# Kernel tuning notes

Measured on AMD Instinct MI355X. Metric: run time of the kernel, lower is better.

Reference implementation:

```python
import jax, jax.numpy as jnp
import numpy as np

STEP_SIZE = 0.3333
MAX_STEPS = 8          # >= ceil(max(2*sigma)/step); extra iterations have k==0 (no-op)
TANGENT_DIRECTION = True


def _bilinear_sample(img, p):
    # img: [B,C,H,W], p: [B,2,H,W] normalized coords in [0,1] (x=width, y=height)
    B, C, H, W = img.shape
    fx = p[:, 0] * W - 0.5   # [B,H,W] pixel-center convention
    fy = p[:, 1] * H - 0.5
    x0 = jnp.floor(fx)
    y0 = jnp.floor(fy)
    wx = (fx - x0)[:, None]  # [B,1,H,W]
    wy = (fy - y0)[:, None]
    x0i = jnp.clip(x0.astype(jnp.int32), 0, W - 1)
    x1i = jnp.clip(x0i + 1, 0, W - 1)
    y0i = jnp.clip(y0.astype(jnp.int32), 0, H - 1)
    y1i = jnp.clip(y0i + 1, 0, H - 1)
    gather = jax.vmap(lambda im, yi, xi: im[:, yi, xi])  # per-batch gather -> [B,C,H,W]
    v00 = gather(img, y0i, x0i)
    v01 = gather(img, y0i, x1i)
    v10 = gather(img, y1i, x0i)
    v11 = gather(img, y1i, x1i)
    return (v00 * (1 - wx) + v01 * wx) * (1 - wy) + (v10 * (1 - wx) + v11 * wx) * wy


def _p_start(H, W, dtype):
    xs = (jnp.arange(W, dtype=dtype) + 0.5) / W
    ys = (jnp.arange(H, dtype=dtype) + 0.5) / H
    px = jnp.broadcast_to(xs[None, :], (H, W))
    py = jnp.broadcast_to(ys[:, None], (H, W))
    return jnp.stack([px, py])[None]  # [1,2,H,W]


def _perp(t):
    return jnp.concatenate([t[:, 1:2], -t[:, 0:1]], axis=1)


def _forward(x, tangent, sigma):
    B, C, H, W = x.shape
    dt = x.dtype
    factor = min(H, W) / 1024.0          # input_size_factor relative to 1024 base res
    sigma = sigma * factor               # [B,1,1,1]
    half_width = 2.0 * sigma
    two_sigma2 = 2.0 * sigma * sigma
    step = jnp.asarray(1.0 / (STEP_SIZE * factor), dtype=dt)
    tex = jnp.array([W, H], dtype=dt).reshape(1, 2, 1, 1)
    p0 = _p_start(H, W, dt)

    def one_pass(direction):
        v = direction if TANGENT_DIRECTION else _perp(direction)
        p = p0 + v / tex
        r = jnp.broadcast_to(step, (B, 1, 1, 1))
        c = jnp.zeros_like(x)
        s = jnp.zeros((B, 1, H, W), dt)

        def body(carry, _):
            c, s, v, p, r = carry
            k = jnp.exp(-r * r / two_sigma2)                 # [B,1,1,1]
            k = jnp.where(r < half_width, k, 0.0)
            inb = ((p[:, 0:1] >= 0.0) & (p[:, 0:1] < 1.0) &
                   (p[:, 1:2] >= 0.0) & (p[:, 1:2] < 1.0))   # [B,1,H,W]
            k = jnp.where(inb, k, 0.0)                        # [B,1,H,W]
            c = c + _bilinear_sample(x, p) * k
            s = s + k
            tf = _bilinear_sample(tangent, p)                 # [B,2,H,W]
            if not TANGENT_DIRECTION:
                tf = _perp(tf)
            vt = jnp.sum(v * tf, axis=1, keepdims=True)
            tf = jnp.where(vt < 0.0, -tf, tf)                 # keep marching direction coherent
            return (c, s, tf, p + tf / tex, r + step), None

        (c, s, _, _, _), _ = jax.lax.scan(body, (c, s, v, p, r), None, length=MAX_STEPS)
        return c, s

    c1, s1 = one_pass(tangent)
    c2, s2 = one_pass(-tangent)
    return (x + c1 + c2) / (1.0 + s1 + s2)


def setup_inputs() -> dict:
    key = jax.random.key(0)
    k1, k2, k3 = jax.random.split(key, 3)
    B, C, H, W = 2, 3, 1024, 1024
    x = jax.random.uniform(k1, (B, C, H, W), dtype=jnp.float32)
    t = jax.random.normal(k2, (B, 2, H, W), dtype=jnp.float32)
    t = t / (jnp.sqrt(jnp.sum(t * t, axis=1, keepdims=True)) + 1e-6)  # unit tangent field
    sigma = 2.0 + 4.0 * jax.random.uniform(k3, (B, 1, 1, 1), dtype=jnp.float32)
    return {"x": x, "tangent": t, "sigma": sigma}


def reference(x, tangent, sigma):
    return _forward(x, tangent, sigma)
```

## Files before the change

### kernel.cpp

```cpp
#include <hip/hip_runtime.h>
#include <hip/hip_fp16.h>


#define HH 1024
#define WW 1024
#define CC 3
#define BB 2
#define NPIX (HH * WW)

#define TS 32
#define HALO_LO 5
#define NWIN 43
#define NREC (NWIN * NWIN)

__device__ __forceinline__ unsigned pk_f16x2(float a, float b) {
    __half2 h = __floats2half2_rn(a, b);
    return *(const unsigned*)&h;
}
__device__ __forceinline__ float2 unpk_f16x2(unsigned u) {
    __half2 h = *(const __half2*)&u;
    return __half22float2(h);
}

template <bool BORDER>
__device__ __forceinline__ float4 march_pixel(
    const uint4* __restrict__ win, int win_x0, int win_y0,
    int ix, int iy, float t0x, float t0y,
    float half_width, float inv_two_sigma2, float step)
{
    const float invT = 1.0f / 1024.0f;
    float acc0 = 0.f, acc1 = 0.f, acc2 = 0.f, accs = 0.f;

    float vx[2], vy[2], px[2], py[2];
    vx[0] = t0x;  vy[0] = t0y;
    vx[1] = -t0x; vy[1] = -t0y;
    const float p0x = ((float)ix + 0.5f) * invT;
    const float p0y = ((float)iy + 0.5f) * invT;
    px[0] = p0x + vx[0] * invT;  py[0] = p0y + vy[0] * invT;
    px[1] = p0x + vx[1] * invT;  py[1] = p0y + vy[1] * invT;

    float r = step;
    for (int it = 0; it < 8; ++it) {
        if (!(r < half_width)) break;
        const float k = __expf(-r * r * inv_two_sigma2);

        #pragma unroll
        for (int c = 0; c < 2; ++c) {
            const float fx = px[c] * 1024.0f - 0.5f;
            const float fy = py[c] * 1024.0f - 0.5f;
            const float x0f = floorf(fx);
            const float y0f = floorf(fy);
            const float wx = fx - x0f;
            const float wy = fy - y0f;

            int jx0, jx1, jy0, jy1;
            if (BORDER) {
                int x0i = (int)x0f, y0i = (int)y0f;
                x0i = min(max(x0i, 0), WW - 1);
                y0i = min(max(y0i, 0), HH - 1);
                const int x1i = min(x0i + 1, WW - 1);
                const int y1i = min(y0i + 1, HH - 1);
                jx0 = x0i - win_x0; jx1 = x1i - win_x0;
                jy0 = y0i - win_y0; jy1 = y1i - win_y0;
            } else {
                jx0 = (int)x0f - win_x0; jx1 = jx0 + 1;
                jy0 = (int)y0f - win_y0; jy1 = jy0 + 1;
            }

            const uint4 q00 = win[jy0 * NWIN + jx0];
            const uint4 q01 = win[jy0 * NWIN + jx1];
            const uint4 q10 = win[jy1 * NWIN + jx0];
            const uint4 q11 = win[jy1 * NWIN + jx1];

            const float wxm = 1.f - wx;
            const float wym = 1.f - wy;
            const float w00 = wxm * wym, w01 = wx * wym;
            const float w10 = wxm * wy,  w11 = wx * wy;

            float tfx = __uint_as_float(q00.x) * w00 + __uint_as_float(q01.x) * w01
                      + __uint_as_float(q10.x) * w10 + __uint_as_float(q11.x) * w11;
            float tfy = __uint_as_float(q00.y) * w00 + __uint_as_float(q01.y) * w01
                      + __uint_as_float(q10.y) * w10 + __uint_as_float(q11.y) * w11;

            bool inb = true;
            if (BORDER)
                inb = (px[c] >= 0.f) && (px[c] < 1.f) &&
                      (py[c] >= 0.f) && (py[c] < 1.f);
            if (inb) {
                const float2 a00 = unpk_f16x2(q00.z);
                const float2 a01 = unpk_f16x2(q01.z);
                const float2 a10 = unpk_f16x2(q10.z);
                const float2 a11 = unpk_f16x2(q11.z);
                const float2 b00 = unpk_f16x2(q00.w);
                const float2 b01 = unpk_f16x2(q01.w);
                const float2 b10 = unpk_f16x2(q10.w);
                const float2 b11 = unpk_f16x2(q11.w);
                acc0 += k * (a00.x * w00 + a01.x * w01 + a10.x * w10 + a11.x * w11);
                acc1 += k * (a00.y * w00 + a01.y * w01 + a10.y * w10 + a11.y * w11);
                acc2 += k * (b00.x * w00 + b01.x * w01 + b10.x * w10 + b11.x * w11);
                accs += k;
            }

            const float vt = vx[c] * tfx + vy[c] * tfy;
            if (vt < 0.f) { tfx = -tfx; tfy = -tfy; }
            vx[c] = tfx; vy[c] = tfy;
            px[c] += tfx * invT;
            py[c] += tfy * invT;
        }
        r += step;
    }
    return make_float4(acc0, acc1, acc2, accs);
}

__global__ __launch_bounds__(256) void flow_smooth_lds32(
    const float* __restrict__ x, const float* __restrict__ tng,
    const float* __restrict__ sigma, float* __restrict__ out)
{
    __shared__ uint4 win[NREC];

    const int b = blockIdx.z;
    const int tile_x0 = blockIdx.x * TS;
    const int tile_y0 = blockIdx.y * TS;
    const int win_x0 = tile_x0 - HALO_LO;
    const int win_y0 = tile_y0 - HALO_LO;

    const float* __restrict__ xb  = x   + (size_t)b * CC * NPIX;
    const float* __restrict__ tbx = tng + (size_t)b * 2 * NPIX;
    const float* __restrict__ tby = tbx + NPIX;

    for (int j = threadIdx.x; j < NREC; j += 256) {
        const int jy = j / NWIN;
        const int jx = j - jy * NWIN;
        const int gy = min(max(win_y0 + jy, 0), HH - 1);
        const int gx = min(max(win_x0 + jx, 0), WW - 1);
        const int g  = gy * WW + gx;
        uint4 rec;
        rec.x = __float_as_uint(tbx[g]);
        rec.y = __float_as_uint(tby[g]);
        rec.z = pk_f16x2(xb[g], xb[NPIX + g]);
        rec.w = pk_f16x2(xb[2 * NPIX + g], 0.0f);
        win[j] = rec;
    }
    __syncthreads();

    const float sig = sigma[b];
    const float half_width = 2.0f * sig;
    const float inv_two_sigma2 = 1.0f / (2.0f * sig * sig);
    const float step = (float)(1.0 / 0.3333);

    const int tx  = threadIdx.x & 31;
    const int ty0 = threadIdx.x >> 5;
    float* __restrict__ ob = out + (size_t)b * CC * NPIX;

    const bool border = (blockIdx.x == 0) | (blockIdx.x == gridDim.x - 1) |
                        (blockIdx.y == 0) | (blockIdx.y == gridDim.y - 1);

    if (!border) {
        #pragma unroll
        for (int q = 0; q < 4; ++q) {
            const int ly = ty0 + 8 * q;
            const int ix = tile_x0 + tx;
            const int iy = tile_y0 + ly;
            const uint4 own = win[(ly + HALO_LO) * NWIN + (tx + HALO_LO)];
            const float t0x = __uint_as_float(own.x);
            const float t0y = __uint_as_float(own.y);
            const float2 c01 = unpk_f16x2(own.z);
            const float2 c2p = unpk_f16x2(own.w);
            const float4 a = march_pixel<false>(win, win_x0, win_y0, ix, iy,
                                                t0x, t0y, half_width,
                                                inv_two_sigma2, step);
            const float inv_den = 1.0f / (1.0f + a.w);
            const int pix = iy * WW + ix;
            ob[pix]            = (c01.x + a.x) * inv_den;
            ob[NPIX + pix]     = (c01.y + a.y) * inv_den;
            ob[2 * NPIX + pix] = (c2p.x + a.z) * inv_den;
        }
    } else {
        #pragma unroll
        for (int q = 0; q < 4; ++q) {
            const int ly = ty0 + 8 * q;
            const int ix = tile_x0 + tx;
            const int iy = tile_y0 + ly;
            const uint4 own = win[(ly + HALO_LO) * NWIN + (tx + HALO_LO)];
            const float t0x = __uint_as_float(own.x);
            const float t0y = __uint_as_float(own.y);
            const float2 c01 = unpk_f16x2(own.z);
            const float2 c2p = unpk_f16x2(own.w);
            const float4 a = march_pixel<true>(win, win_x0, win_y0, ix, iy,
                                               t0x, t0y, half_width,
                                               inv_two_sigma2, step);
            const float inv_den = 1.0f / (1.0f + a.w);
            const int pix = iy * WW + ix;
            ob[pix]            = (c01.x + a.x) * inv_den;
            ob[NPIX + pix]     = (c01.y + a.y) * inv_den;
            ob[2 * NPIX + pix] = (c2p.x + a.z) * inv_den;
        }
    }
}

extern "C" void kernel_launch(void* const* d_in, const int* in_sizes, int n_in,
                              void* d_out, int out_size, void* d_ws, size_t ws_size,
                              hipStream_t stream) {
    const float* x  = (const float*)d_in[0];
    const float* t  = (const float*)d_in[1];
    const float* sg = (const float*)d_in[2];
    float* out = (float*)d_out;

    dim3 grid(WW / TS, HH / TS, BB);
    flow_smooth_lds32<<<grid, dim3(256), 0, stream>>>(x, t, sg, out);
}
```

Baseline: 123.0 us.

## Use packed fp16 bilinear color math, pixel-space coords, 512-thread blocks

Does the color bilinear interpolation with packed half2 FMAs and switches positions from normalized to pixel units, dropping the scale multiplies. Tangent interpolation is restructured into separable lerps with explicit round-to-nearest mul/add, likely to stay close to the reference rounding. Blocks grow to 512 threads with 2 pixels per thread, and the border/interior branch moves inside the loop. This aims to cut ALU work per step and raise occupancy, at the cost of fp16 precision in the color accumulation and the blocked FMA contraction in the tangent path.

```diff
diff --git a/kernel.cpp b/kernel.cpp
--- a/kernel.cpp
+++ b/kernel.cpp
@@ -17,10 +17,11 @@
     __half2 h = __floats2half2_rn(a, b);
     return *(const unsigned*)&h;
 }
-__device__ __forceinline__ float2 unpk_f16x2(unsigned u) {
-    __half2 h = *(const __half2*)&u;
-    return __half22float2(h);
-}
+__device__ __forceinline__ __half2 u2h(unsigned u) {
+    return *(const __half2*)&u;
+}
+__device__ __forceinline__ float mrn(float a, float b) { return __fmul_rn(a, b); }
+__device__ __forceinline__ float arn(float a, float b) { return __fadd_rn(a, b); }
 
 template <bool BORDER>
 __device__ __forceinline__ float4 march_pixel(
@@ -28,16 +29,17 @@
     int ix, int iy, float t0x, float t0y,
     float half_width, float inv_two_sigma2, float step)
 {
-    const float invT = 1.0f / 1024.0f;
+    const __half2 h2one = __float2half2_rn(1.0f);
+
     float acc0 = 0.f, acc1 = 0.f, acc2 = 0.f, accs = 0.f;
 
-    float vx[2], vy[2], px[2], py[2];
+    float vx[2], vy[2], Px[2], Py[2];
     vx[0] = t0x;  vy[0] = t0y;
     vx[1] = -t0x; vy[1] = -t0y;
-    const float p0x = ((float)ix + 0.5f) * invT;
-    const float p0y = ((float)iy + 0.5f) * invT;
-    px[0] = p0x + vx[0] * invT;  py[0] = p0y + vy[0] * invT;
-    px[1] = p0x + vx[1] * invT;  py[1] = p0y + vy[1] * invT;
+    const float P0x = (float)ix + 0.5f;
+    const float P0y = (float)iy + 0.5f;
+    Px[0] = arn(P0x, vx[0]);  Py[0] = arn(P0y, vy[0]);
+    Px[1] = arn(P0x, vx[1]);  Py[1] = arn(P0y, vy[1]);
 
     float r = step;
     for (int it = 0; it < 8; ++it) {
@@ -46,73 +48,78 @@
 
         #pragma unroll
         for (int c = 0; c < 2; ++c) {
-            const float fx = px[c] * 1024.0f - 0.5f;
-            const float fy = py[c] * 1024.0f - 0.5f;
+            const float fx = Px[c] - 0.5f;
+            const float fy = Py[c] - 0.5f;
             const float x0f = floorf(fx);
             const float y0f = floorf(fy);
             const float wx = fx - x0f;
             const float wy = fy - y0f;
 
-            int jx0, jx1, jy0, jy1;
-            if (BORDER) {
-                int x0i = (int)x0f, y0i = (int)y0f;
+            uint4 q00, q01, q10, q11;
+            if (!BORDER) {
+                const int jx0 = (int)x0f - win_x0;
+                const int jy0 = (int)y0f - win_y0;
+                const uint4* q = win + (jy0 * NWIN + jx0);
+                q00 = q[0]; q01 = q[1]; q10 = q[NWIN]; q11 = q[NWIN + 1];
+            } else {
+                int x0i = (int)x0f;
+                int y0i = (int)y0f;
                 x0i = min(max(x0i, 0), WW - 1);
                 y0i = min(max(y0i, 0), HH - 1);
                 const int x1i = min(x0i + 1, WW - 1);
                 const int y1i = min(y0i + 1, HH - 1);
-                jx0 = x0i - win_x0; jx1 = x1i - win_x0;
-                jy0 = y0i - win_y0; jy1 = y1i - win_y0;
-            } else {
-                jx0 = (int)x0f - win_x0; jx1 = jx0 + 1;
-                jy0 = (int)y0f - win_y0; jy1 = jy0 + 1;
+                const int jx0 = x0i - win_x0, jx1 = x1i - win_x0;
+                const int jy0 = y0i - win_y0, jy1 = y1i - win_y0;
+                q00 = win[jy0 * NWIN + jx0];
+                q01 = win[jy0 * NWIN + jx1];
+                q10 = win[jy1 * NWIN + jx0];
+                q11 = win[jy1 * NWIN + jx1];
             }
-
-            const uint4 q00 = win[jy0 * NWIN + jx0];
-            const uint4 q01 = win[jy0 * NWIN + jx1];
-            const uint4 q10 = win[jy1 * NWIN + jx0];
-            const uint4 q11 = win[jy1 * NWIN + jx1];
 
             const float wxm = 1.f - wx;
             const float wym = 1.f - wy;
-            const float w00 = wxm * wym, w01 = wx * wym;
-            const float w10 = wxm * wy,  w11 = wx * wy;
-
-            float tfx = __uint_as_float(q00.x) * w00 + __uint_as_float(q01.x) * w01
-                      + __uint_as_float(q10.x) * w10 + __uint_as_float(q11.x) * w11;
-            float tfy = __uint_as_float(q00.y) * w00 + __uint_as_float(q01.y) * w01
-                      + __uint_as_float(q10.y) * w10 + __uint_as_float(q11.y) * w11;
+
+            const float rx0 = arn(mrn(__uint_as_float(q00.x), wxm), mrn(__uint_as_float(q01.x), wx));
+            const float rx1 = arn(mrn(__uint_as_float(q10.x), wxm), mrn(__uint_as_float(q11.x), wx));
+            const float ry0 = arn(mrn(__uint_as_float(q00.y), wxm), mrn(__uint_as_float(q01.y), wx));
+            const float ry1 = arn(mrn(__uint_as_float(q10.y), wxm), mrn(__uint_as_float(q11.y), wx));
+            float tfx = arn(mrn(rx0, wym), mrn(rx1, wy));
+            float tfy = arn(mrn(ry0, wym), mrn(ry1, wy));
 
             bool inb = true;
             if (BORDER)
-                inb = (px[c] >= 0.f) && (px[c] < 1.f) &&
-                      (py[c] >= 0.f) && (py[c] < 1.f);
+                inb = (Px[c] >= 0.f) && (Px[c] < 1024.f) &&
+                      (Py[c] >= 0.f) && (Py[c] < 1024.f);
             if (inb) {
-                const float2 a00 = unpk_f16x2(q00.z);
-                const float2 a01 = unpk_f16x2(q01.z);
-                const float2 a10 = unpk_f16x2(q10.z);
-                const float2 a11 = unpk_f16x2(q11.z);
-                const float2 b00 = unpk_f16x2(q00.w);
-                const float2 b01 = unpk_f16x2(q01.w);
-                const float2 b10 = unpk_f16x2(q10.w);
-                const float2 b11 = unpk_f16x2(q11.w);
-                acc0 += k * (a00.x * w00 + a01.x * w01 + a10.x * w10 + a11.x * w11);
-                acc1 += k * (a00.y * w00 + a01.y * w01 + a10.y * w10 + a11.y * w11);
-                acc2 += k * (b00.x * w00 + b01.x * w01 + b10.x * w10 + b11.x * w11);
+                const __half2 hwx  = __float2half2_rn(wx);
+                const __half2 hwy  = __float2half2_rn(wy);
+                const __half2 hwxm = __hsub2(h2one, hwx);
+                const __half2 hwym = __hsub2(h2one, hwy);
+                const __half2 az0 = __hfma2(u2h(q01.z), hwx, __hmul2(u2h(q00.z), hwxm));
+                const __half2 az1 = __hfma2(u2h(q11.z), hwx, __hmul2(u2h(q10.z), hwxm));
+                const __half2 az  = __hfma2(az1, hwy, __hmul2(az0, hwym));
+                const __half2 aw0 = __hfma2(u2h(q01.w), hwx, __hmul2(u2h(q00.w), hwxm));
+                const __half2 aw1 = __hfma2(u2h(q11.w), hwx, __hmul2(u2h(q10.w), hwxm));
+                const __half2 aw  = __hfma2(aw1, hwy, __hmul2(aw0, hwym));
+                const float2 f01 = __half22float2(az);
+                acc0 = fmaf(k, f01.x, acc0);
+                acc1 = fmaf(k, f01.y, acc1);
+                acc2 = fmaf(k, __low2float(aw), acc2);
                 accs += k;
             }
 
-            const float vt = vx[c] * tfx + vy[c] * tfy;
+            const float vt = arn(mrn(vx[c], tfx), mrn(vy[c], tfy));
             if (vt < 0.f) { tfx = -tfx; tfy = -tfy; }
             vx[c] = tfx; vy[c] = tfy;
-            px[c] += tfx * invT;
-            py[c] += tfy * invT;
+            Px[c] = arn(Px[c], tfx);
+            Py[c] = arn(Py[c], tfy);
         }
         r += step;
     }
     return make_float4(acc0, acc1, acc2, accs);
 }
 
-__global__ __launch_bounds__(256) void flow_smooth_lds32(
+__global__ __launch_bounds__(512, 8) void flow_smooth_r9(
     const float* __restrict__ x, const float* __restrict__ tng,
     const float* __restrict__ sigma, float* __restrict__ out)
 {
@@ -128,7 +135,7 @@
     const float* __restrict__ tbx = tng + (size_t)b * 2 * NPIX;
     const float* __restrict__ tby = tbx + NPIX;
 
-    for (int j = threadIdx.x; j < NREC; j += 256) {
+    for (int j = threadIdx.x; j < NREC; j += 512) {
         const int jy = j / NWIN;
         const int jx = j - jy * NWIN;
         const int gy = min(max(win_y0 + jy, 0), HH - 1);
@@ -155,46 +162,30 @@
     const bool border = (blockIdx.x == 0) | (blockIdx.x == gridDim.x - 1) |
                         (blockIdx.y == 0) | (blockIdx.y == gridDim.y - 1);
 
-    if (!border) {
-        #pragma unroll
-        for (int q = 0; q < 4; ++q) {
-            const int ly = ty0 + 8 * q;
-            const int ix = tile_x0 + tx;
-            const int iy = tile_y0 + ly;
-            const uint4 own = win[(ly + HALO_LO) * NWIN + (tx + HALO_LO)];
-            const float t0x = __uint_as_float(own.x);
-            const float t0y = __uint_as_float(own.y);
-            const float2 c01 = unpk_f16x2(own.z);
-            const float2 c2p = unpk_f16x2(own.w);
-            const float4 a = march_pixel<false>(win, win_x0, win_y0, ix, iy,
-                                                t0x, t0y, half_width,
-                                                inv_two_sigma2, step);
-            const float inv_den = 1.0f / (1.0f + a.w);
-            const int pix = iy * WW + ix;
-            ob[pix]            = (c01.x + a.x) * inv_den;
-            ob[NPIX + pix]     = (c01.y + a.y) * inv_den;
-            ob[2 * NPIX + pix] = (c2p.x + a.z) * inv_den;
-        }
-    } else {
-        #pragma unroll
-        for (int q = 0; q < 4; ++q) {
-            const int ly = ty0 + 8 * q;
-            const int ix = tile_x0 + tx;
-            const int iy = tile_y0 + ly;
-            const uint4 own = win[(ly + HALO_LO) * NWIN + (tx + HALO_LO)];
-            const float t0x = __uint_as_float(own.x);
-            const float t0y = __uint_as_float(own.y);
-            const float2 c01 = unpk_f16x2(own.z);
-            const float2 c2p = unpk_f16x2(own.w);
-            const float4 a = march_pixel<true>(win, win_x0, win_y0, ix, iy,
-                                               t0x, t0y, half_width,
-                                               inv_two_sigma2, step);
-            const float inv_den = 1.0f / (1.0f + a.w);
-            const int pix = iy * WW + ix;
-            ob[pix]            = (c01.x + a.x) * inv_den;
-            ob[NPIX + pix]     = (c01.y + a.y) * inv_den;
-            ob[2 * NPIX + pix] = (c2p.x + a.z) * inv_den;
-        }
+    #pragma unroll
+    for (int q = 0; q < 2; ++q) {
+        const int ly = ty0 + 16 * q;
+        const int ix = tile_x0 + tx;
+        const int iy = tile_y0 + ly;
+        const uint4 own = win[(ly + HALO_LO) * NWIN + (tx + HALO_LO)];
+        const float t0x = __uint_as_float(own.x);
+        const float t0y = __uint_as_float(own.y);
+        const float2 c01 = __half22float2(u2h(own.z));
+        const float  c2  = __low2float(u2h(own.w));
+
+        float4 a;
+        if (!border)
+            a = march_pixel<false>(win, win_x0, win_y0, ix, iy, t0x, t0y,
+                                   half_width, inv_two_sigma2, step);
+        else
+            a = march_pixel<true>(win, win_x0, win_y0, ix, iy, t0x, t0y,
+                                  half_width, inv_two_sigma2, step);
+
+        const float inv_den = 1.0f / (1.0f + a.w);
+        const int pix = iy * WW + ix;
+        ob[pix]            = (c01.x + a.x) * inv_den;
+        ob[NPIX + pix]     = (c01.y + a.y) * inv_den;
+        ob[2 * NPIX + pix] = (c2   + a.z) * inv_den;
     }
 }
 
@@ -207,5 +198,5 @@
     float* out = (float*)d_out;
 
     dim3 grid(WW / TS, HH / TS, BB);
-    flow_smooth_lds32<<<grid, dim3(256), 0, stream>>>(x, t, sg, out);
-}
+    flow_smooth_r9<<<grid, dim3(512), 0, stream>>>(x, t, sg, out);
+}
```

Result: slower. 126.7 us (+3.0%).
